# Performance work log

Measured on AMD Instinct MI355X. Metric: run time of the kernel, lower is better.

## Reference

```python
import math
import jax, jax.numpy as jnp
import numpy as np

NUM_HEADS = 8
HEAD_DIM = 64


def setup_inputs() -> dict:
    key = jax.random.key(0)
    k1, k2, k3, k4 = jax.random.split(key, 4)
    C = 256
    E = NUM_HEADS * HEAD_DIM  # 512
    x = jax.random.normal(k1, (4, C, 48, 48), dtype=jnp.float32)
    Wqkv = jax.random.normal(k2, (3 * E, C), dtype=jnp.float32) * (1.0 / math.sqrt(C))
    Wout = jax.random.normal(k3, (C, E), dtype=jnp.float32) * (1.0 / math.sqrt(E))
    bout = jax.random.normal(k4, (C,), dtype=jnp.float32) * 0.01
    return {"x": x, "Wqkv": Wqkv, "Wout": Wout, "bout": bout}


def reference(x, Wqkv, Wout, bout):
    b, c, H, W = x.shape
    nh, hd = NUM_HEADS, HEAD_DIM
    N = H * W
    scale = 1.0 / math.sqrt(hd)
    # 1x1 conv (no bias) == channel matmul
    qkv = jnp.einsum('bcxy,oc->boxy', x, Wqkv)            # [b, 3*nh*hd, H, W]
    qkv = qkv.reshape(b, 3, nh, hd, N)                    # channel split order: (k, h, d)
    q, k, v = qkv[:, 0], qkv[:, 1], qkv[:, 2]             # each [b, nh, hd, N]
    att = jnp.einsum('bhdi,bhdj->bhij', q, k) * scale     # [b, nh, N, N]
    att = jax.nn.softmax(att, axis=-1)                    # stable (max-subtract inside)
    out = jnp.einsum('bhij,bhdj->bhid', att, v)           # [b, nh, N, hd]
    out = out.transpose(0, 1, 3, 2).reshape(b, nh * hd, H, W)  # 'b h (x y) d -> b (h d) x y'
    # 1x1 conv with bias
    return jnp.einsum('bexy,ce->bcxy', out, Wout) + bout[None, :, None, None]
```

## Files before the change

### kernel.cpp

```cpp
#include <hip/hip_runtime.h>

typedef __attribute__((ext_vector_type(8))) __bf16 bf16x8;
typedef __attribute__((ext_vector_type(16))) float f32x16;
typedef __attribute__((ext_vector_type(4))) float f32x4;
typedef __attribute__((ext_vector_type(4))) unsigned short us4;

__device__ __forceinline__ unsigned short f2bf(float f) {
  __bf16 h = (__bf16)f;
  return __builtin_bit_cast(unsigned short, h);
}
__device__ __forceinline__ unsigned pack2bf(float lo, float hi) {
  return (unsigned)f2bf(lo) | ((unsigned)f2bf(hi) << 16);
}

#define GLL(src, dst)                                                            \
  __builtin_amdgcn_global_load_lds((const __attribute__((address_space(1))) void*)(src), \
                                   (__attribute__((address_space(3))) void*)(dst), 16, 0, 0)

__device__ __forceinline__ void stage_chunks(const unsigned short* g, int ld,
                                             unsigned short* lds, int rows, int tid) {
  int total = rows * 8;
  for (int c0 = 0; c0 < total; c0 += 256) {
    int c = c0 + tid;
    int row = c >> 3, kc = c & 7;
    const unsigned short* src = g + (size_t)row * ld + ((kc ^ (row & 7)) << 3);
    unsigned short* dst = lds + (size_t)(c0 + (tid & 192)) * 8;
    GLL(src, dst);
  }
}

__device__ __forceinline__ bf16x8 frag(const unsigned short* lds, int row, int kc) {
  return *(const bf16x8*)(lds + row * 64 + ((kc ^ (row & 7)) << 3));
}


__global__ void k_cvt(const float* __restrict__ in, unsigned short* __restrict__ outp, int n) {
  int i = (blockIdx.x * 256 + threadIdx.x) * 4;
  if (i + 3 < n) {
    f32x4 v = *(const f32x4*)(in + i);
    us4 o;
#pragma unroll
    for (int k = 0; k < 4; k++) o[k] = f2bf(v[k]);
    *(us4*)(outp + i) = o;
  }
}

__global__ __launch_bounds__(256) void k_xpose(const float* __restrict__ x,
                                               unsigned short* __restrict__ xT) {
  __shared__ float t[32][33];
  int tid = threadIdx.x;
  int col = tid & 31, rowb = tid >> 5;
  int nt = blockIdx.x * 32, ct = blockIdx.y * 32, b = blockIdx.z;
  const float* src = x + ((size_t)b * 256 + ct) * 2304 + nt;
#pragma unroll
  for (int rr = 0; rr < 32; rr += 8) t[rowb + rr][col] = src[(size_t)(rowb + rr) * 2304 + col];
  __syncthreads();
  unsigned short* dst = xT + ((size_t)b * 2304 + nt) * 256 + ct;
#pragma unroll
  for (int rr = 0; rr < 32; rr += 8) dst[(size_t)(rowb + rr) * 256 + col] = f2bf(t[col][rowb + rr]);
}

__global__ __launch_bounds__(256, 2) void k_gemm_qkv(
    const unsigned short* __restrict__ W, const unsigned short* __restrict__ xT,
    unsigned short* __restrict__ qT, unsigned short* __restrict__ kT,
    unsigned short* __restrict__ vv) {
  __shared__ unsigned short As[128 * 64];
  __shared__ unsigned short Bs[128 * 64];
  int tid = threadIdx.x, lane = tid & 63, wid = tid >> 6;
  int m0 = blockIdx.x * 128, n0 = blockIdx.y * 128, b = blockIdx.z;
  const unsigned short* Ag = W + (size_t)m0 * 256;
  const unsigned short* Bg = xT + ((size_t)b * 2304 + n0) * 256;
  int wm = (wid >> 1) * 64, wn = (wid & 1) * 64;
  f32x4 acc[4][4] = {};
  for (int kt = 0; kt < 256; kt += 64) {
    __syncthreads();
    stage_chunks(Ag + kt, 256, As, 128, tid);
    stage_chunks(Bg + kt, 256, Bs, 128, tid);
    __syncthreads();
#pragma unroll
    for (int kk = 0; kk < 2; kk++) {
      bf16x8 af[4], bf[4];
#pragma unroll
      for (int i = 0; i < 4; i++) af[i] = frag(As, wm + i * 16 + (lane & 15), kk * 4 + (lane >> 4));
#pragma unroll
      for (int j = 0; j < 4; j++) bf[j] = frag(Bs, wn + j * 16 + (lane & 15), kk * 4 + (lane >> 4));
#pragma unroll
      for (int i = 0; i < 4; i++)
#pragma unroll
        for (int j = 0; j < 4; j++)
          acc[i][j] = __builtin_amdgcn_mfma_f32_16x16x32_bf16(af[i], bf[j], acc[i][j], 0, 0, 0);
    }
  }
#pragma unroll
  for (int i = 0; i < 4; i++) {
    int o = m0 + wm + i * 16 + ((lane >> 4) << 2);
    int which = o >> 9, h = (o >> 6) & 7, d0 = o & 63;
#pragma unroll
    for (int j = 0; j < 4; j++) {
      int n = n0 + wn + j * 16 + (lane & 15);
      if (which == 2) {
#pragma unroll
        for (int jj = 0; jj < 4; jj++)
          vv[((size_t)(b * 8 + h) * 64 + d0 + jj) * 2304 + n] = f2bf(acc[i][j][jj]);
      } else {
        float sc = which ? 1.0f : 0.18033688011112042f;
        us4 pk;
#pragma unroll
        for (int jj = 0; jj < 4; jj++) pk[jj] = f2bf(acc[i][j][jj] * sc);
        unsigned short* dst = (which ? kT : qT) + ((size_t)(b * 8 + h) * 2304 + n) * 64 + d0;
        *(us4*)dst = pk;
      }
    }
  }
}

__global__ __launch_bounds__(256, 2) void k_attn(
    const unsigned short* __restrict__ qT, const unsigned short* __restrict__ kT,
    const unsigned short* __restrict__ vv, unsigned short* __restrict__ o2T) {
  __shared__ unsigned short L[2][4][4096];
  int tid = threadIdx.x, lane = tid & 63;
  int wid = tid >> 6, rh = wid & 1, jh = wid >> 1;
  int il = lane & 31, g = lane >> 5;
  int lin = blockIdx.x;
  int xcd = lin & 7, idx = lin >> 3;
  int bh = xcd * 4 + idx / 36;
  int i0 = (idx % 36) * 64;
  const unsigned short* kT_bh = kT + (size_t)bh * 2304 * 64;
  const unsigned short* vv_bh = vv + (size_t)bh * 64 * 2304;
  const unsigned short* qrow = qT + ((size_t)bh * 2304 + i0 + rh * 32 + il) * 64;
  bf16x8 qf[4];
#pragma unroll
  for (int ks = 0; ks < 4; ks++) qf[ks] = *(const bf16x8*)(qrow + (ks * 2 + g) * 8);

  int cA = tid, cB = tid + 256;
  int rA = cA >> 3, rB = cB >> 3;
  unsigned swA = (unsigned)(((cA & 7) ^ (rA & 7)) << 3);
  unsigned swB = (unsigned)(((cB & 7) ^ (rB & 7)) << 3);
  unsigned oKA = rA * 64 + swA, oKB = rB * 64 + swB;
  unsigned oVA = rA * 2304 + swA, oVB = rB * 2304 + swB;
  int db = (tid & 192) * 8;
  unsigned short* dKA0 = &L[0][0][db];
  unsigned short* dKB0 = &L[0][0][2048 + db];
  unsigned short* dKA1 = &L[0][1][db];
  unsigned short* dKB1 = &L[0][1][2048 + db];
  unsigned short* dVA0 = &L[0][2][db];
  unsigned short* dVB0 = &L[0][2][2048 + db];
  unsigned short* dVA1 = &L[0][3][db];
  unsigned short* dVB1 = &L[0][3][2048 + db];

#define STAGE(boff)                                  \
  do {                                               \
    GLL(kT_bh + oKA, dKA0 + (boff));                 \
    GLL(kT_bh + oKB, dKB0 + (boff));                 \
    GLL(kT_bh + 73728 + oKA, dKA1 + (boff));         \
    GLL(kT_bh + 73728 + oKB, dKB1 + (boff));         \
    GLL(vv_bh + oVA, dVA0 + (boff));                 \
    GLL(vv_bh + oVB, dVB0 + (boff));                 \
    GLL(vv_bh + 1152 + oVA, dVA1 + (boff));          \
    GLL(vv_bh + 1152 + oVB, dVB1 + (boff));          \
    oKA += 4096; oKB += 4096; oVA += 64; oVB += 64;  \
  } while (0)

  const unsigned short* fK[8];
  const unsigned short* fV[8];
#pragma unroll
  for (int ks = 0; ks < 4; ks++) {
    int cs = ks * 2 + g;
    int o0 = il * 64 + ((cs ^ (il & 7)) << 3);
    int o1 = (32 + il) * 64 + ((cs ^ (il & 7)) << 3);
    fK[ks] = &L[0][jh][o0];
    fK[4 + ks] = &L[0][jh][o1];
    fV[ks] = &L[0][2 + jh][o0];
    fV[4 + ks] = &L[0][2 + jh][o1];
  }

  float lrun = 0.f;
  f32x16 O0 = {}, O1 = {};

#define COMP(boff)                                                                        \
  do {                                                                                    \
    f32x16 S0 = {}, S1 = {};                                                              \
    _Pragma("unroll") for (int ks = 0; ks < 4; ks++) {                                    \
      bf16x8 kf0 = *(const bf16x8*)(fK[ks] + (boff));                                     \
      bf16x8 kf1 = *(const bf16x8*)(fK[4 + ks] + (boff));                                 \
      S0 = __builtin_amdgcn_mfma_f32_32x32x16_bf16(kf0, qf[ks], S0, 0, 0, 0);             \
      S1 = __builtin_amdgcn_mfma_f32_32x32x16_bf16(kf1, qf[ks], S1, 0, 0, 0);             \
    }                                                                                     \
    float a16[16];                                                                        \
    _Pragma("unroll") for (int r = 0; r < 16; r++) {                                      \
      S0[r] = __builtin_amdgcn_exp2f(S0[r]);                                              \
      S1[r] = __builtin_amdgcn_exp2f(S1[r]);                                              \
      a16[r] = S0[r] + S1[r];                                                             \
    }                                                                                     \
    _Pragma("unroll") for (int s = 8; s >= 1; s >>= 1)                                    \
        _Pragma("unroll") for (int r = 0; r < 8; r++) if (r < s) a16[r] += a16[r + s];    \
    lrun += a16[0];                                                                       \
    unsigned w0[8], w1[8];                                                                \
    _Pragma("unroll") for (int m = 0; m < 8; m++) {                                       \
      w0[m] = pack2bf(S0[2 * m], S0[2 * m + 1]);                                          \
      w1[m] = pack2bf(S1[2 * m], S1[2 * m + 1]);                                          \
    }                                                                                     \
    _Pragma("unroll") for (int ks = 0; ks < 4; ks++) {                                    \
      int a = ks & 1;                                                                     \
      unsigned A0, A1, B0, B1;                                                            \
      if (ks >> 1) { A0 = w1[4 * a]; A1 = w1[4 * a + 1]; B0 = w1[4 * a + 2]; B1 = w1[4 * a + 3]; } \
      else         { A0 = w0[4 * a]; A1 = w0[4 * a + 1]; B0 = w0[4 * a + 2]; B1 = w0[4 * a + 3]; } \
      unsigned send0 = g ? A0 : B0, send1 = g ? A1 : B1;                                  \
      unsigned pw0 = __shfl_xor(send0, 32), pw1 = __shfl_xor(send1, 32);                  \
      union { unsigned u[4]; bf16x8 v; } F;                                               \
      F.u[0] = g ? pw0 : A0;                                                              \
      F.u[1] = g ? pw1 : A1;                                                              \
      F.u[2] = g ? B0 : pw0;                                                              \
      F.u[3] = g ? B1 : pw1;                                                              \
      bf16x8 vf0 = *(const bf16x8*)(fV[ks] + (boff));                                     \
      bf16x8 vf1 = *(const bf16x8*)(fV[4 + ks] + (boff));                                 \
      O0 = __builtin_amdgcn_mfma_f32_32x32x16_bf16(vf0, F.v, O0, 0, 0, 0);                \
      O1 = __builtin_amdgcn_mfma_f32_32x32x16_bf16(vf1, F.v, O1, 0, 0, 0);                \
    }                                                                                     \
  } while (0)

  STAGE(0);
  __syncthreads();
#pragma unroll 1
  for (int it = 0; it < 9; it++) {
    STAGE(16384);
    COMP(0);
    __syncthreads();
    if (it < 8) STAGE(0);
    COMP(16384);
    __syncthreads();
  }
#undef STAGE
#undef COMP

  lrun += __shfl_xor(lrun, 32);
  float* sm = (float*)&L[0][0][0];
  float* ml = (float*)&L[1][0][0];
  if (jh == 1) {
#pragma unroll
    for (int r = 0; r < 16; r++) {
      sm[(rh * 32 + r) * 64 + lane] = O0[r];
      sm[(rh * 32 + 16 + r) * 64 + lane] = O1[r];
    }
    if (!g) ml[rh * 32 + il] = lrun;
  }
  __syncthreads();
  if (jh == 0) {
    float rl = 1.0f / (lrun + ml[rh * 32 + il]);
    int b = bh >> 3, h = bh & 7;
    unsigned short* dst = o2T + ((size_t)b * 2304 + (i0 + rh * 32 + il)) * 512 + h * 64;
#pragma unroll
    for (int dt = 0; dt < 2; dt++) {
#pragma unroll
      for (int u = 0; u < 4; u++) {
        us4 pk;
#pragma unroll
        for (int v = 0; v < 4; v++) {
          int r = 4 * u + v;
          float own = dt ? O1[r] : O0[r];
          float oth = sm[(rh * 32 + dt * 16 + r) * 64 + lane];
          pk[v] = f2bf((own + oth) * rl);
        }
        *(us4*)(dst + dt * 32 + 8 * u + 4 * g) = pk;
      }
    }
  }
}

__global__ __launch_bounds__(256, 2) void k_gemm_out(
    const unsigned short* __restrict__ Wo, const unsigned short* __restrict__ o2T,
    const float* __restrict__ bout, float* __restrict__ out) {
  __shared__ unsigned short As[128 * 64];
  __shared__ unsigned short Bs[128 * 64];
  int tid = threadIdx.x, lane = tid & 63, wid = tid >> 6;
  int m0 = blockIdx.x * 128, n0 = blockIdx.y * 128, b = blockIdx.z;
  const unsigned short* Ag = Wo + (size_t)m0 * 512;
  const unsigned short* Bg = o2T + ((size_t)b * 2304 + n0) * 512;
  int wm = (wid >> 1) * 64, wn = (wid & 1) * 64;
  f32x4 acc[4][4] = {};
  for (int kt = 0; kt < 512; kt += 64) {
    __syncthreads();
    stage_chunks(Ag + kt, 512, As, 128, tid);
    stage_chunks(Bg + kt, 512, Bs, 128, tid);
    __syncthreads();
#pragma unroll
    for (int kk = 0; kk < 2; kk++) {
      bf16x8 af[4], bf[4];
#pragma unroll
      for (int i = 0; i < 4; i++) af[i] = frag(As, wm + i * 16 + (lane & 15), kk * 4 + (lane >> 4));
#pragma unroll
      for (int j = 0; j < 4; j++) bf[j] = frag(Bs, wn + j * 16 + (lane & 15), kk * 4 + (lane >> 4));
#pragma unroll
      for (int i = 0; i < 4; i++)
#pragma unroll
        for (int j = 0; j < 4; j++)
          acc[i][j] = __builtin_amdgcn_mfma_f32_16x16x32_bf16(af[i], bf[j], acc[i][j], 0, 0, 0);
    }
  }
#pragma unroll
  for (int i = 0; i < 4; i++) {
    int c = m0 + wm + i * 16 + ((lane >> 4) << 2);
#pragma unroll
    for (int j = 0; j < 4; j++) {
      int n = n0 + wn + j * 16 + (lane & 15);
#pragma unroll
      for (int jj = 0; jj < 4; jj++)
        out[((size_t)b * 256 + c + jj) * 2304 + n] = acc[i][j][jj] + bout[c + jj];
    }
  }
}

extern "C" void kernel_launch(void* const* d_in, const int* in_sizes, int n_in,
                              void* d_out, int out_size, void* d_ws, size_t ws_size,
                              hipStream_t stream) {
  const float* x = (const float*)d_in[0];
  const float* Wqkv = (const float*)d_in[1];
  const float* Wout = (const float*)d_in[2];
  const float* bout = (const float*)d_in[3];
  float* out = (float*)d_out;
  char* ws = (char*)d_ws;
  unsigned short* Wqkv_bf = (unsigned short*)(ws + 0);
  unsigned short* Wout_bf = (unsigned short*)(ws + 786432);
  unsigned short* xT      = (unsigned short*)(ws + 1048576);
  unsigned short* qT      = (unsigned short*)(ws + 5767168);
  unsigned short* kT      = (unsigned short*)(ws + 15204352);
  unsigned short* vv      = (unsigned short*)(ws + 24641536);
  unsigned short* o2T     = (unsigned short*)(ws + 34078720);

  k_cvt<<<dim3(384), dim3(256), 0, stream>>>(Wqkv, Wqkv_bf, 1536 * 256);
  k_cvt<<<dim3(128), dim3(256), 0, stream>>>(Wout, Wout_bf, 256 * 512);
  k_xpose<<<dim3(72, 8, 4), dim3(256), 0, stream>>>(x, xT);
  k_gemm_qkv<<<dim3(12, 18, 4), dim3(256), 0, stream>>>(Wqkv_bf, xT, qT, kT, vv);
  k_attn<<<dim3(1152), dim3(256), 0, stream>>>(qT, kT, vv, o2T);
  k_gemm_out<<<dim3(2, 18, 4), dim3(256), 0, stream>>>(Wout_bf, o2T, bout, out);
}
```

Before: 113.1 us.

## Double attention query tile per block and raise MFMA wave priority

The attention kernel now runs 512-thread blocks that each cover 128 query rows with eight waves, so each staged K/V tile in LDS serves twice as many query rows. Each thread issues half as many global-to-LDS loads, and the grid shrinks to 576 blocks. The MFMA sections are also wrapped in s_setprio so waves doing matrix work get scheduling priority over the exp/pack phase. The risk is that __launch_bounds__(512, 4) squeezes the register budget hard enough to cause spills, and the wider block shifts the LDS and occupancy balance.

```diff
diff --git a/kernel.cpp b/kernel.cpp
--- a/kernel.cpp
+++ b/kernel.cpp
@@ -114,17 +114,17 @@
   }
 }
 
-__global__ __launch_bounds__(256, 2) void k_attn(
+__global__ __launch_bounds__(512, 4) void k_attn(
     const unsigned short* __restrict__ qT, const unsigned short* __restrict__ kT,
     const unsigned short* __restrict__ vv, unsigned short* __restrict__ o2T) {
   __shared__ unsigned short L[2][4][4096];
   int tid = threadIdx.x, lane = tid & 63;
-  int wid = tid >> 6, rh = wid & 1, jh = wid >> 1;
+  int wid = tid >> 6, rh = wid & 3, jh = wid >> 2;
   int il = lane & 31, g = lane >> 5;
   int lin = blockIdx.x;
   int xcd = lin & 7, idx = lin >> 3;
-  int bh = xcd * 4 + idx / 36;
-  int i0 = (idx % 36) * 64;
+  int bh = xcd * 4 + idx / 18;
+  int i0 = (idx % 18) * 128;
   const unsigned short* kT_bh = kT + (size_t)bh * 2304 * 64;
   const unsigned short* vv_bh = vv + (size_t)bh * 64 * 2304;
   const unsigned short* qrow = qT + ((size_t)bh * 2304 + i0 + rh * 32 + il) * 64;
@@ -132,33 +132,23 @@
 #pragma unroll
   for (int ks = 0; ks < 4; ks++) qf[ks] = *(const bf16x8*)(qrow + (ks * 2 + g) * 8);
 
-  int cA = tid, cB = tid + 256;
-  int rA = cA >> 3, rB = cB >> 3;
-  unsigned swA = (unsigned)(((cA & 7) ^ (rA & 7)) << 3);
-  unsigned swB = (unsigned)(((cB & 7) ^ (rB & 7)) << 3);
-  unsigned oKA = rA * 64 + swA, oKB = rB * 64 + swB;
-  unsigned oVA = rA * 2304 + swA, oVB = rB * 2304 + swB;
-  int db = (tid & 192) * 8;
-  unsigned short* dKA0 = &L[0][0][db];
-  unsigned short* dKB0 = &L[0][0][2048 + db];
-  unsigned short* dKA1 = &L[0][1][db];
-  unsigned short* dKB1 = &L[0][1][2048 + db];
-  unsigned short* dVA0 = &L[0][2][db];
-  unsigned short* dVB0 = &L[0][2][2048 + db];
-  unsigned short* dVA1 = &L[0][3][db];
-  unsigned short* dVB1 = &L[0][3][2048 + db];
-
-#define STAGE(boff)                                  \
-  do {                                               \
-    GLL(kT_bh + oKA, dKA0 + (boff));                 \
-    GLL(kT_bh + oKB, dKB0 + (boff));                 \
-    GLL(kT_bh + 73728 + oKA, dKA1 + (boff));         \
-    GLL(kT_bh + 73728 + oKB, dKB1 + (boff));         \
-    GLL(vv_bh + oVA, dVA0 + (boff));                 \
-    GLL(vv_bh + oVB, dVB0 + (boff));                 \
-    GLL(vv_bh + 1152 + oVA, dVA1 + (boff));          \
-    GLL(vv_bh + 1152 + oVB, dVB1 + (boff));          \
-    oKA += 4096; oKB += 4096; oVA += 64; oVB += 64;  \
+  int srow = tid >> 3, skc = tid & 7;
+  unsigned sw = (unsigned)((skc ^ (srow & 7)) << 3);
+  unsigned oK = srow * 64 + sw;
+  unsigned oV = srow * 2304 + sw;
+  int db = (tid & 448) * 8;
+  unsigned short* dK0 = &L[0][0][db];
+  unsigned short* dK1 = &L[0][1][db];
+  unsigned short* dV0 = &L[0][2][db];
+  unsigned short* dV1 = &L[0][3][db];
+
+#define STAGE(boff)                          \
+  do {                                       \
+    GLL(kT_bh + oK, dK0 + (boff));           \
+    GLL(kT_bh + 73728 + oK, dK1 + (boff));   \
+    GLL(vv_bh + oV, dV0 + (boff));           \
+    GLL(vv_bh + 1152 + oV, dV1 + (boff));    \
+    oK += 4096; oV += 64;                    \
   } while (0)
 
   const unsigned short* fK[8];
@@ -180,12 +170,14 @@
 #define COMP(boff)                                                                        \
   do {                                                                                    \
     f32x16 S0 = {}, S1 = {};                                                              \
+    __builtin_amdgcn_s_setprio(1);                                                        \
     _Pragma("unroll") for (int ks = 0; ks < 4; ks++) {                                    \
       bf16x8 kf0 = *(const bf16x8*)(fK[ks] + (boff));                                     \
       bf16x8 kf1 = *(const bf16x8*)(fK[4 + ks] + (boff));                                 \
       S0 = __builtin_amdgcn_mfma_f32_32x32x16_bf16(kf0, qf[ks], S0, 0, 0, 0);             \
       S1 = __builtin_amdgcn_mfma_f32_32x32x16_bf16(kf1, qf[ks], S1, 0, 0, 0);             \
     }                                                                                     \
+    __builtin_amdgcn_s_setprio(0);                                                        \
     float a16[16];                                                                        \
     _Pragma("unroll") for (int r = 0; r < 16; r++) {                                      \
       S0[r] = __builtin_amdgcn_exp2f(S0[r]);                                              \
@@ -200,6 +192,7 @@
       w0[m] = pack2bf(S0[2 * m], S0[2 * m + 1]);                                          \
       w1[m] = pack2bf(S1[2 * m], S1[2 * m + 1]);                                          \
     }                                                                                     \
+    __builtin_amdgcn_s_setprio(1);                                                        \
     _Pragma("unroll") for (int ks = 0; ks < 4; ks++) {                                    \
       int a = ks & 1;                                                                     \
       unsigned A0, A1, B0, B1;                                                            \
@@ -217,6 +210,7 @@
       O0 = __builtin_amdgcn_mfma_f32_32x32x16_bf16(vf0, F.v, O0, 0, 0, 0);                \
       O1 = __builtin_amdgcn_mfma_f32_32x32x16_bf16(vf1, F.v, O1, 0, 0, 0);                \
     }                                                                                     \
+    __builtin_amdgcn_s_setprio(0);                                                        \
   } while (0)
 
   STAGE(0);
@@ -331,6 +325,6 @@
   k_cvt<<<dim3(128), dim3(256), 0, stream>>>(Wout, Wout_bf, 256 * 512);
   k_xpose<<<dim3(72, 8, 4), dim3(256), 0, stream>>>(x, xT);
   k_gemm_qkv<<<dim3(12, 18, 4), dim3(256), 0, stream>>>(Wqkv_bf, xT, qT, kT, vv);
-  k_attn<<<dim3(1152), dim3(256), 0, stream>>>(qT, kT, vv, o2T);
+  k_attn<<<dim3(576), dim3(512), 0, stream>>>(qT, kT, vv, o2T);
   k_gemm_out<<<dim3(2, 18, 4), dim3(256), 0, stream>>>(Wout_bf, o2T, bout, out);
 }
```

Result: no change. 111.5 us (-1.4%).

## Double attention query tile per block to reuse staged K/V fragments

Applied to the files above, without the earlier changes.

Each attention block now handles 128 query rows instead of 64, so every wave computes two 32-row query sub-tiles against the same K and V fragments read from LDS. This halves the grid to 576 blocks and halves the total K/V global-to-LDS staging traffic. It also adds s_setprio around the MFMA bursts to favour matrix issue. In exchange, register pressure roughly doubles for the accumulators and the grid becomes smaller relative to the CU count, which may cut occupancy and wave-level parallelism.

```diff
diff --git a/kernel.cpp b/kernel.cpp
--- a/kernel.cpp
+++ b/kernel.cpp
@@ -123,14 +123,20 @@
   int il = lane & 31, g = lane >> 5;
   int lin = blockIdx.x;
   int xcd = lin & 7, idx = lin >> 3;
-  int bh = xcd * 4 + idx / 36;
-  int i0 = (idx % 36) * 64;
+  int bh = xcd * 4 + idx / 18;
+  int i0 = (idx % 18) * 128;
   const unsigned short* kT_bh = kT + (size_t)bh * 2304 * 64;
   const unsigned short* vv_bh = vv + (size_t)bh * 64 * 2304;
-  const unsigned short* qrow = qT + ((size_t)bh * 2304 + i0 + rh * 32 + il) * 64;
-  bf16x8 qf[4];
-#pragma unroll
-  for (int ks = 0; ks < 4; ks++) qf[ks] = *(const bf16x8*)(qrow + (ks * 2 + g) * 8);
+  bf16x8 qfA[4], qfB[4];
+  {
+    const unsigned short* qrowA = qT + ((size_t)bh * 2304 + i0 + rh * 64 + il) * 64;
+    const unsigned short* qrowB = qrowA + 32 * 64;
+#pragma unroll
+    for (int ks = 0; ks < 4; ks++) {
+      qfA[ks] = *(const bf16x8*)(qrowA + (ks * 2 + g) * 8);
+      qfB[ks] = *(const bf16x8*)(qrowB + (ks * 2 + g) * 8);
+    }
+  }
 
   int cA = tid, cB = tid + 256;
   int rA = cA >> 3, rB = cB >> 3;
@@ -174,49 +180,67 @@
     fV[4 + ks] = &L[0][2 + jh][o1];
   }
 
-  float lrun = 0.f;
-  f32x16 O0 = {}, O1 = {};
-
-#define COMP(boff)                                                                        \
-  do {                                                                                    \
-    f32x16 S0 = {}, S1 = {};                                                              \
-    _Pragma("unroll") for (int ks = 0; ks < 4; ks++) {                                    \
-      bf16x8 kf0 = *(const bf16x8*)(fK[ks] + (boff));                                     \
-      bf16x8 kf1 = *(const bf16x8*)(fK[4 + ks] + (boff));                                 \
-      S0 = __builtin_amdgcn_mfma_f32_32x32x16_bf16(kf0, qf[ks], S0, 0, 0, 0);             \
-      S1 = __builtin_amdgcn_mfma_f32_32x32x16_bf16(kf1, qf[ks], S1, 0, 0, 0);             \
-    }                                                                                     \
-    float a16[16];                                                                        \
-    _Pragma("unroll") for (int r = 0; r < 16; r++) {                                      \
-      S0[r] = __builtin_amdgcn_exp2f(S0[r]);                                              \
-      S1[r] = __builtin_amdgcn_exp2f(S1[r]);                                              \
-      a16[r] = S0[r] + S1[r];                                                             \
-    }                                                                                     \
-    _Pragma("unroll") for (int s = 8; s >= 1; s >>= 1)                                    \
-        _Pragma("unroll") for (int r = 0; r < 8; r++) if (r < s) a16[r] += a16[r + s];    \
-    lrun += a16[0];                                                                       \
-    unsigned w0[8], w1[8];                                                                \
-    _Pragma("unroll") for (int m = 0; m < 8; m++) {                                       \
-      w0[m] = pack2bf(S0[2 * m], S0[2 * m + 1]);                                          \
-      w1[m] = pack2bf(S1[2 * m], S1[2 * m + 1]);                                          \
-    }                                                                                     \
-    _Pragma("unroll") for (int ks = 0; ks < 4; ks++) {                                    \
-      int a = ks & 1;                                                                     \
-      unsigned A0, A1, B0, B1;                                                            \
+  float lrunA = 0.f, lrunB = 0.f;
+  f32x16 OA0 = {}, OA1 = {}, OB0 = {}, OB1 = {};
+
+#define SOFTMAX_PACK(S0, S1, lsum, w0, w1)                                              \
+  do {                                                                                  \
+    float a16[16];                                                                      \
+    _Pragma("unroll") for (int r = 0; r < 16; r++) {                                    \
+      S0[r] = __builtin_amdgcn_exp2f(S0[r]);                                            \
+      S1[r] = __builtin_amdgcn_exp2f(S1[r]);                                            \
+      a16[r] = S0[r] + S1[r];                                                           \
+    }                                                                                   \
+    _Pragma("unroll") for (int s = 8; s >= 1; s >>= 1)                                  \
+        _Pragma("unroll") for (int r = 0; r < 8; r++) if (r < s) a16[r] += a16[r + s];  \
+    lsum += a16[0];                                                                     \
+    _Pragma("unroll") for (int m = 0; m < 8; m++) {                                     \
+      w0[m] = pack2bf(S0[2 * m], S0[2 * m + 1]);                                        \
+      w1[m] = pack2bf(S1[2 * m], S1[2 * m + 1]);                                        \
+    }                                                                                   \
+  } while (0)
+
+#define PV(w0, w1, O0, O1, vf)                                                          \
+  do {                                                                                  \
+    _Pragma("unroll") for (int ks = 0; ks < 4; ks++) {                                  \
+      int a = ks & 1;                                                                   \
+      unsigned A0, A1, B0, B1;                                                          \
       if (ks >> 1) { A0 = w1[4 * a]; A1 = w1[4 * a + 1]; B0 = w1[4 * a + 2]; B1 = w1[4 * a + 3]; } \
       else         { A0 = w0[4 * a]; A1 = w0[4 * a + 1]; B0 = w0[4 * a + 2]; B1 = w0[4 * a + 3]; } \
-      unsigned send0 = g ? A0 : B0, send1 = g ? A1 : B1;                                  \
-      unsigned pw0 = __shfl_xor(send0, 32), pw1 = __shfl_xor(send1, 32);                  \
-      union { unsigned u[4]; bf16x8 v; } F;                                               \
-      F.u[0] = g ? pw0 : A0;                                                              \
-      F.u[1] = g ? pw1 : A1;                                                              \
-      F.u[2] = g ? B0 : pw0;                                                              \
-      F.u[3] = g ? B1 : pw1;                                                              \
-      bf16x8 vf0 = *(const bf16x8*)(fV[ks] + (boff));                                     \
-      bf16x8 vf1 = *(const bf16x8*)(fV[4 + ks] + (boff));                                 \
-      O0 = __builtin_amdgcn_mfma_f32_32x32x16_bf16(vf0, F.v, O0, 0, 0, 0);                \
-      O1 = __builtin_amdgcn_mfma_f32_32x32x16_bf16(vf1, F.v, O1, 0, 0, 0);                \
-    }                                                                                     \
+      unsigned send0 = g ? A0 : B0, send1 = g ? A1 : B1;                                \
+      unsigned pw0 = __shfl_xor(send0, 32), pw1 = __shfl_xor(send1, 32);                \
+      union { unsigned u[4]; bf16x8 v; } F;                                             \
+      F.u[0] = g ? pw0 : A0;                                                            \
+      F.u[1] = g ? pw1 : A1;                                                            \
+      F.u[2] = g ? B0 : pw0;                                                            \
+      F.u[3] = g ? B1 : pw1;                                                            \
+      O0 = __builtin_amdgcn_mfma_f32_32x32x16_bf16(vf[ks], F.v, O0, 0, 0, 0);           \
+      O1 = __builtin_amdgcn_mfma_f32_32x32x16_bf16(vf[4 + ks], F.v, O1, 0, 0, 0);       \
+    }                                                                                   \
+  } while (0)
+
+#define COMP(boff)                                                                      \
+  do {                                                                                  \
+    bf16x8 kf[8];                                                                       \
+    _Pragma("unroll") for (int q = 0; q < 8; q++) kf[q] = *(const bf16x8*)(fK[q] + (boff)); \
+    f32x16 SA0 = {}, SA1 = {}, SB0 = {}, SB1 = {};                                      \
+    __builtin_amdgcn_s_setprio(1);                                                      \
+    _Pragma("unroll") for (int ks = 0; ks < 4; ks++) {                                  \
+      SA0 = __builtin_amdgcn_mfma_f32_32x32x16_bf16(kf[ks], qfA[ks], SA0, 0, 0, 0);     \
+      SA1 = __builtin_amdgcn_mfma_f32_32x32x16_bf16(kf[4 + ks], qfA[ks], SA1, 0, 0, 0); \
+      SB0 = __builtin_amdgcn_mfma_f32_32x32x16_bf16(kf[ks], qfB[ks], SB0, 0, 0, 0);     \
+      SB1 = __builtin_amdgcn_mfma_f32_32x32x16_bf16(kf[4 + ks], qfB[ks], SB1, 0, 0, 0); \
+    }                                                                                   \
+    __builtin_amdgcn_s_setprio(0);                                                      \
+    unsigned wA0[8], wA1[8], wB0[8], wB1[8];                                            \
+    SOFTMAX_PACK(SA0, SA1, lrunA, wA0, wA1);                                            \
+    SOFTMAX_PACK(SB0, SB1, lrunB, wB0, wB1);                                            \
+    bf16x8 vf[8];                                                                       \
+    _Pragma("unroll") for (int q = 0; q < 8; q++) vf[q] = *(const bf16x8*)(fV[q] + (boff)); \
+    __builtin_amdgcn_s_setprio(1);                                                      \
+    PV(wA0, wA1, OA0, OA1, vf);                                                         \
+    PV(wB0, wB1, OB0, OB1, vf);                                                         \
+    __builtin_amdgcn_s_setprio(0);                                                      \
   } while (0)
 
   STAGE(0);
@@ -232,36 +256,49 @@
   }
 #undef STAGE
 #undef COMP
-
-  lrun += __shfl_xor(lrun, 32);
+#undef SOFTMAX_PACK
+#undef PV
+
+  lrunA += __shfl_xor(lrunA, 32);
+  lrunB += __shfl_xor(lrunB, 32);
   float* sm = (float*)&L[0][0][0];
   float* ml = (float*)&L[1][0][0];
   if (jh == 1) {
 #pragma unroll
     for (int r = 0; r < 16; r++) {
-      sm[(rh * 32 + r) * 64 + lane] = O0[r];
-      sm[(rh * 32 + 16 + r) * 64 + lane] = O1[r];
-    }
-    if (!g) ml[rh * 32 + il] = lrun;
+      sm[((rh * 2 + 0) * 32 + r) * 64 + lane] = OA0[r];
+      sm[((rh * 2 + 0) * 32 + 16 + r) * 64 + lane] = OA1[r];
+      sm[((rh * 2 + 1) * 32 + r) * 64 + lane] = OB0[r];
+      sm[((rh * 2 + 1) * 32 + 16 + r) * 64 + lane] = OB1[r];
+    }
+    if (!g) {
+      ml[(rh * 2 + 0) * 32 + il] = lrunA;
+      ml[(rh * 2 + 1) * 32 + il] = lrunB;
+    }
   }
   __syncthreads();
   if (jh == 0) {
-    float rl = 1.0f / (lrun + ml[rh * 32 + il]);
     int b = bh >> 3, h = bh & 7;
-    unsigned short* dst = o2T + ((size_t)b * 2304 + (i0 + rh * 32 + il)) * 512 + h * 64;
-#pragma unroll
-    for (int dt = 0; dt < 2; dt++) {
-#pragma unroll
-      for (int u = 0; u < 4; u++) {
-        us4 pk;
-#pragma unroll
-        for (int v = 0; v < 4; v++) {
-          int r = 4 * u + v;
-          float own = dt ? O1[r] : O0[r];
-          float oth = sm[(rh * 32 + dt * 16 + r) * 64 + lane];
-          pk[v] = f2bf((own + oth) * rl);
+#pragma unroll
+    for (int qb = 0; qb < 2; qb++) {
+      float lr = qb ? lrunB : lrunA;
+      float rl = 1.0f / (lr + ml[(rh * 2 + qb) * 32 + il]);
+      unsigned short* dst =
+          o2T + ((size_t)b * 2304 + (i0 + rh * 64 + qb * 32 + il)) * 512 + h * 64;
+#pragma unroll
+      for (int dt = 0; dt < 2; dt++) {
+#pragma unroll
+        for (int u = 0; u < 4; u++) {
+          us4 pk;
+#pragma unroll
+          for (int v = 0; v < 4; v++) {
+            int r = 4 * u + v;
+            float own = qb ? (dt ? OB1[r] : OB0[r]) : (dt ? OA1[r] : OA0[r]);
+            float oth = sm[((rh * 2 + qb) * 32 + dt * 16 + r) * 64 + lane];
+            pk[v] = f2bf((own + oth) * rl);
+          }
+          *(us4*)(dst + dt * 32 + 8 * u + 4 * g) = pk;
         }
-        *(us4*)(dst + dt * 32 + 8 * u + 4 * g) = pk;
       }
     }
   }
@@ -331,6 +368,6 @@
   k_cvt<<<dim3(128), dim3(256), 0, stream>>>(Wout, Wout_bf, 256 * 512);
   k_xpose<<<dim3(72, 8, 4), dim3(256), 0, stream>>>(x, xT);
   k_gemm_qkv<<<dim3(12, 18, 4), dim3(256), 0, stream>>>(Wqkv_bf, xT, qT, kT, vv);
-  k_attn<<<dim3(1152), dim3(256), 0, stream>>>(qT, kT, vv, o2T);
+  k_attn<<<dim3(576), dim3(256), 0, stream>>>(qT, kT, vv, o2T);
   k_gemm_out<<<dim3(2, 18, 4), dim3(256), 0, stream>>>(Wout_bf, o2T, bout, out);
 }
```

Measured after the change: 116.6 us. +3.1%, slower.

## Halve per-iteration KV tile in attention kernel to raise occupancy

Applied to the files above, without the earlier changes.

Each loop iteration of the attention kernel now stages 64 keys instead of 128, which halves the LDS buffer. Each jh wave-half handles 32 keys, with the V fragment pointers remapped to match. Launch bounds go from 2 to 4 blocks per CU, and s_setprio is wrapped around the MFMA sections. The aim is more resident waves to hide latency, at the cost of twice as many iterations and barriers and fewer independent MFMA chains per wave.

```diff
diff --git a/kernel.cpp b/kernel.cpp
--- a/kernel.cpp
+++ b/kernel.cpp
@@ -114,10 +114,10 @@
   }
 }
 
-__global__ __launch_bounds__(256, 2) void k_attn(
+__global__ __launch_bounds__(256, 4) void k_attn(
     const unsigned short* __restrict__ qT, const unsigned short* __restrict__ kT,
     const unsigned short* __restrict__ vv, unsigned short* __restrict__ o2T) {
-  __shared__ unsigned short L[2][4][4096];
+  __shared__ unsigned short L[2][2][4096];
   int tid = threadIdx.x, lane = tid & 63;
   int wid = tid >> 6, rh = wid & 1, jh = wid >> 1;
   int il = lane & 31, g = lane >> 5;
@@ -139,95 +139,84 @@
   unsigned oKA = rA * 64 + swA, oKB = rB * 64 + swB;
   unsigned oVA = rA * 2304 + swA, oVB = rB * 2304 + swB;
   int db = (tid & 192) * 8;
-  unsigned short* dKA0 = &L[0][0][db];
-  unsigned short* dKB0 = &L[0][0][2048 + db];
-  unsigned short* dKA1 = &L[0][1][db];
-  unsigned short* dKB1 = &L[0][1][2048 + db];
-  unsigned short* dVA0 = &L[0][2][db];
-  unsigned short* dVB0 = &L[0][2][2048 + db];
-  unsigned short* dVA1 = &L[0][3][db];
-  unsigned short* dVB1 = &L[0][3][2048 + db];
-
-#define STAGE(boff)                                  \
-  do {                                               \
-    GLL(kT_bh + oKA, dKA0 + (boff));                 \
-    GLL(kT_bh + oKB, dKB0 + (boff));                 \
-    GLL(kT_bh + 73728 + oKA, dKA1 + (boff));         \
-    GLL(kT_bh + 73728 + oKB, dKB1 + (boff));         \
-    GLL(vv_bh + oVA, dVA0 + (boff));                 \
-    GLL(vv_bh + oVB, dVB0 + (boff));                 \
-    GLL(vv_bh + 1152 + oVA, dVA1 + (boff));          \
-    GLL(vv_bh + 1152 + oVB, dVB1 + (boff));          \
-    oKA += 4096; oKB += 4096; oVA += 64; oVB += 64;  \
+  unsigned short* dKA = &L[0][0][db];
+  unsigned short* dKB = &L[0][0][2048 + db];
+  unsigned short* dVA = &L[0][1][db];
+  unsigned short* dVB = &L[0][1][2048 + db];
+
+#define STAGE(boff)                          \
+  do {                                       \
+    GLL(kT_bh + oKA, dKA + (boff));          \
+    GLL(kT_bh + oKB, dKB + (boff));          \
+    GLL(vv_bh + oVA, dVA + (boff));          \
+    GLL(vv_bh + oVB, dVB + (boff));          \
+    oKA += 4096; oKB += 4096; oVA += 64; oVB += 64; \
   } while (0)
 
-  const unsigned short* fK[8];
-  const unsigned short* fV[8];
+  const unsigned short* fK[4];
+  const unsigned short* fV[4];
 #pragma unroll
   for (int ks = 0; ks < 4; ks++) {
     int cs = ks * 2 + g;
-    int o0 = il * 64 + ((cs ^ (il & 7)) << 3);
-    int o1 = (32 + il) * 64 + ((cs ^ (il & 7)) << 3);
-    fK[ks] = &L[0][jh][o0];
-    fK[4 + ks] = &L[0][jh][o1];
-    fV[ks] = &L[0][2 + jh][o0];
-    fV[4 + ks] = &L[0][2 + jh][o1];
-  }
+    fK[ks] = &L[0][0][(jh * 32 + il) * 64 + ((cs ^ (il & 7)) << 3)];
+  }
+#pragma unroll
+  for (int ks = 0; ks < 2; ks++)
+#pragma unroll
+    for (int dblk = 0; dblk < 2; dblk++) {
+      int cs = jh * 4 + ks * 2 + g;
+      fV[ks * 2 + dblk] = &L[0][1][(dblk * 32 + il) * 64 + ((cs ^ (il & 7)) << 3)];
+    }
 
   float lrun = 0.f;
   f32x16 O0 = {}, O1 = {};
 
-#define COMP(boff)                                                                        \
-  do {                                                                                    \
-    f32x16 S0 = {}, S1 = {};                                                              \
-    _Pragma("unroll") for (int ks = 0; ks < 4; ks++) {                                    \
-      bf16x8 kf0 = *(const bf16x8*)(fK[ks] + (boff));                                     \
-      bf16x8 kf1 = *(const bf16x8*)(fK[4 + ks] + (boff));                                 \
-      S0 = __builtin_amdgcn_mfma_f32_32x32x16_bf16(kf0, qf[ks], S0, 0, 0, 0);             \
-      S1 = __builtin_amdgcn_mfma_f32_32x32x16_bf16(kf1, qf[ks], S1, 0, 0, 0);             \
-    }                                                                                     \
-    float a16[16];                                                                        \
-    _Pragma("unroll") for (int r = 0; r < 16; r++) {                                      \
-      S0[r] = __builtin_amdgcn_exp2f(S0[r]);                                              \
-      S1[r] = __builtin_amdgcn_exp2f(S1[r]);                                              \
-      a16[r] = S0[r] + S1[r];                                                             \
-    }                                                                                     \
-    _Pragma("unroll") for (int s = 8; s >= 1; s >>= 1)                                    \
-        _Pragma("unroll") for (int r = 0; r < 8; r++) if (r < s) a16[r] += a16[r + s];    \
-    lrun += a16[0];                                                                       \
-    unsigned w0[8], w1[8];                                                                \
-    _Pragma("unroll") for (int m = 0; m < 8; m++) {                                       \
-      w0[m] = pack2bf(S0[2 * m], S0[2 * m + 1]);                                          \
-      w1[m] = pack2bf(S1[2 * m], S1[2 * m + 1]);                                          \
-    }                                                                                     \
-    _Pragma("unroll") for (int ks = 0; ks < 4; ks++) {                                    \
-      int a = ks & 1;                                                                     \
-      unsigned A0, A1, B0, B1;                                                            \
-      if (ks >> 1) { A0 = w1[4 * a]; A1 = w1[4 * a + 1]; B0 = w1[4 * a + 2]; B1 = w1[4 * a + 3]; } \
-      else         { A0 = w0[4 * a]; A1 = w0[4 * a + 1]; B0 = w0[4 * a + 2]; B1 = w0[4 * a + 3]; } \
-      unsigned send0 = g ? A0 : B0, send1 = g ? A1 : B1;                                  \
-      unsigned pw0 = __shfl_xor(send0, 32), pw1 = __shfl_xor(send1, 32);                  \
-      union { unsigned u[4]; bf16x8 v; } F;                                               \
-      F.u[0] = g ? pw0 : A0;                                                              \
-      F.u[1] = g ? pw1 : A1;                                                              \
-      F.u[2] = g ? B0 : pw0;                                                              \
-      F.u[3] = g ? B1 : pw1;                                                              \
-      bf16x8 vf0 = *(const bf16x8*)(fV[ks] + (boff));                                     \
-      bf16x8 vf1 = *(const bf16x8*)(fV[4 + ks] + (boff));                                 \
-      O0 = __builtin_amdgcn_mfma_f32_32x32x16_bf16(vf0, F.v, O0, 0, 0, 0);                \
-      O1 = __builtin_amdgcn_mfma_f32_32x32x16_bf16(vf1, F.v, O1, 0, 0, 0);                \
-    }                                                                                     \
+#define COMP(boff)                                                                      \
+  do {                                                                                  \
+    bf16x8 kf[4];                                                                       \
+    _Pragma("unroll") for (int q = 0; q < 4; q++) kf[q] = *(const bf16x8*)(fK[q] + (boff)); \
+    f32x16 S0 = {};                                                                     \
+    __builtin_amdgcn_s_setprio(1);                                                      \
+    _Pragma("unroll") for (int ks = 0; ks < 4; ks++)                                    \
+      S0 = __builtin_amdgcn_mfma_f32_32x32x16_bf16(kf[ks], qf[ks], S0, 0, 0, 0);        \
+    __builtin_amdgcn_s_setprio(0);                                                      \
+    float a16[16];                                                                      \
+    _Pragma("unroll") for (int r = 0; r < 16; r++) {                                    \
+      S0[r] = __builtin_amdgcn_exp2f(S0[r]);                                            \
+      a16[r] = S0[r];                                                                   \
+    }                                                                                   \
+    _Pragma("unroll") for (int s = 8; s >= 1; s >>= 1)                                  \
+        _Pragma("unroll") for (int r = 0; r < 8; r++) if (r < s) a16[r] += a16[r + s];  \
+    lrun += a16[0];                                                                     \
+    unsigned w[8];                                                                      \
+    _Pragma("unroll") for (int m = 0; m < 8; m++) w[m] = pack2bf(S0[2 * m], S0[2 * m + 1]); \
+    bf16x8 vf[4];                                                                       \
+    _Pragma("unroll") for (int q = 0; q < 4; q++) vf[q] = *(const bf16x8*)(fV[q] + (boff)); \
+    __builtin_amdgcn_s_setprio(1);                                                      \
+    _Pragma("unroll") for (int ks = 0; ks < 2; ks++) {                                  \
+      unsigned A0 = w[4 * ks], A1 = w[4 * ks + 1], B0 = w[4 * ks + 2], B1 = w[4 * ks + 3]; \
+      unsigned send0 = g ? A0 : B0, send1 = g ? A1 : B1;                                \
+      unsigned pw0 = __shfl_xor(send0, 32), pw1 = __shfl_xor(send1, 32);                \
+      union { unsigned u[4]; bf16x8 v; } F;                                             \
+      F.u[0] = g ? pw0 : A0;                                                            \
+      F.u[1] = g ? pw1 : A1;                                                            \
+      F.u[2] = g ? B0 : pw0;                                                            \
+      F.u[3] = g ? B1 : pw1;                                                            \
+      O0 = __builtin_amdgcn_mfma_f32_32x32x16_bf16(vf[ks * 2 + 0], F.v, O0, 0, 0, 0);   \
+      O1 = __builtin_amdgcn_mfma_f32_32x32x16_bf16(vf[ks * 2 + 1], F.v, O1, 0, 0, 0);   \
+    }                                                                                   \
+    __builtin_amdgcn_s_setprio(0);                                                      \
   } while (0)
 
   STAGE(0);
   __syncthreads();
 #pragma unroll 1
-  for (int it = 0; it < 9; it++) {
-    STAGE(16384);
+  for (int it = 0; it < 18; it++) {
+    STAGE(8192);
     COMP(0);
     __syncthreads();
-    if (it < 8) STAGE(0);
-    COMP(16384);
+    if (it < 17) STAGE(0);
+    COMP(8192);
     __syncthreads();
   }
 #undef STAGE
```

Measured after the change: 112.7 us. Within noise of the previous version (-0.4%).
